# Performance work log

Measured on AMD Instinct MI355X. Metric: run time of the kernel, lower is better.

## Reference

```python
import jax, jax.numpy as jnp
import numpy as np
from jax import lax

B, IMG, P, STRIDE, CIN = 4, 256, 8, 8, 1
D, NH, L = 768, 8, 21
GRID = (IMG - P) // STRIDE + 1  # 32
N = GRID * GRID                 # 1024 tokens
HD = D // NH                    # 96
SCALE = float(HD) ** -0.5


def setup_inputs() -> dict:
    key = jax.random.key(0)
    ks = jax.random.split(key, 9)
    s = 0.02
    return {
        "sam": jax.random.normal(ks[0], (B, CIN, IMG, IMG), dtype=jnp.float32),
        "conv_w": jax.random.normal(ks[1], (D, CIN, P, P), dtype=jnp.float32) * s,
        "conv_b": jnp.zeros((D,), dtype=jnp.float32),
        "ln_g": jnp.ones((D,), dtype=jnp.float32),
        "ln_b": jnp.zeros((D,), dtype=jnp.float32),
        "pos": jax.random.normal(ks[2], (N, D), dtype=jnp.float32) * s,
        "q_w": jax.random.normal(ks[3], (L, D, D), dtype=jnp.float32) * s,
        "kv_w": jax.random.normal(ks[4], (L, D, 2 * D), dtype=jnp.float32) * s,
        "proj_w": jax.random.normal(ks[5], (L, D, D), dtype=jnp.float32) * s,
        "proj_b": jnp.zeros((L, D), dtype=jnp.float32),
    }


def _layernorm(x, g, b, eps=1e-5):
    mu = jnp.mean(x, axis=-1, keepdims=True)
    var = jnp.mean(jnp.square(x - mu), axis=-1, keepdims=True)
    return (x - mu) * lax.rsqrt(var + eps) * g + b


def _guidance(x, qw, kvw, pw, pb):
    b, n, c = x.shape
    q = jnp.einsum('bnc,cd->bnd', x, qw).reshape(b, n, NH, HD).transpose(0, 2, 1, 3)
    kv = jnp.einsum('bnc,cd->bnd', x, kvw)
    k = kv[..., :c].reshape(b, n, NH, HD).transpose(0, 2, 1, 3)
    v = kv[..., c:].reshape(b, n, NH, HD).transpose(0, 2, 1, 3)
    attn = jax.nn.softmax(jnp.einsum('bhnd,bhmd->bhnm', q, k) * SCALE, axis=-1)
    o = jnp.einsum('bhnm,bhmd->bhnd', attn, v).transpose(0, 2, 1, 3).reshape(b, n, c)
    o = jnp.einsum('bnc,cd->bnd', o, pw) + pb
    return o + x  # residual (dropouts are identity in eval)


def reference(sam, conv_w, conv_b, ln_g, ln_b, pos, q_w, kv_w, proj_w, proj_b):
    # Patch embed: conv (valid, stride=patch) -> [B,D,32,32] -> tokens -> LN
    y = lax.conv_general_dilated(sam, conv_w, window_strides=(STRIDE, STRIDE),
                                 padding='VALID',
                                 dimension_numbers=('NCHW', 'OIHW', 'NCHW'))
    y = y + conv_b[None, :, None, None]
    y = y.reshape(B, D, N).transpose(0, 2, 1)  # [B,N,D]
    y = _layernorm(y, ln_g, ln_b)
    x0 = y + pos[None]  # pos_embed(arange) broadcast over batch
    # Faithful to source: each block consumes the SAME x0; output is last block's.
    out = x0
    for i in range(L):
        out = _guidance(x0, q_w[i], kv_w[i], proj_w[i], proj_b[i])
    return out
```

## Files before the change

kernel.cpp:

```cpp
#include <hip/hip_runtime.h>
#include <hip/hip_bf16.h>

typedef __attribute__((ext_vector_type(4))) float f32x4;
typedef __attribute__((ext_vector_type(8))) short s16x8;
typedef unsigned short u16;
typedef unsigned int u32;

#define DEV __device__ __forceinline__

DEV u16 f2bf(float f) {
  union { float f; u32 u; } v; v.f = f;
  u32 r = v.u + 0x7fffu + ((v.u >> 16) & 1u);
  return (u16)(r >> 16);
}

#define MFMA16(a, b, c) __builtin_amdgcn_mfma_f32_16x16x32_bf16((a), (b), (c), 0, 0, 0)
#define GLD16(g, l) __builtin_amdgcn_global_load_lds((const __attribute__((address_space(1))) u32*)(g), (__attribute__((address_space(3))) u32*)(l), 16, 0, 0)

#define QSCALE 0.10206207261596577f

__global__ __launch_bounds__(256) void prep_k(
    const float* __restrict__ qw, const float* __restrict__ kvw,
    const float* __restrict__ pw, u16* __restrict__ wqkvT, u16* __restrict__ pwT,
    const float* __restrict__ sam, const float* __restrict__ cw,
    const float* __restrict__ cb, const float* __restrict__ g,
    const float* __restrict__ bb, const float* __restrict__ pos,
    float* __restrict__ x0f, u16* __restrict__ x0b) {
  __shared__ float tb[32][33];
  __shared__ float pix[4][64];
  __shared__ float red[2][4][4];
  int bid = blockIdx.x;
  if (bid < 2304) {
    int ct = bid / 24, kt = (bid % 24) * 32;
    const float* src;
    u16* dst;
    int ncols, tn, dstbase;
    float scale = 1.0f;
    if (ct < 24) {
      src = qw; ncols = 768; tn = ct * 32; dst = wqkvT; dstbase = tn; scale = QSCALE;
    } else if (ct < 72) {
      src = kvw; ncols = 1536; tn = (ct - 24) * 32; dst = wqkvT; dstbase = 768 + tn;
    } else {
      src = pw; ncols = 768; tn = (ct - 72) * 32; dst = pwT; dstbase = tn;
    }
    int tx = threadIdx.x & 31, ty = threadIdx.x >> 5;
#pragma unroll
    for (int i = 0; i < 4; i++)
      tb[ty + i * 8][tx] = src[(size_t)(kt + ty + i * 8) * ncols + tn + tx];
    __syncthreads();
#pragma unroll
    for (int i = 0; i < 4; i++)
      dst[(size_t)(dstbase + ty + i * 8) * 768 + kt + tx] = f2bf(tb[tx][ty + i * 8] * scale);
    return;
  }
  int blk = bid - 2304;
  int b = blk >> 8, nq = blk & 255;
  int t = threadIdx.x;
  {
    int tk = t >> 6, p = t & 63;
    int n = nq * 4 + tk;
    int gi = n >> 5, gj = n & 31;
    pix[tk][p] = sam[b * 65536 + (gi * 8 + (p >> 3)) * 256 + gj * 8 + (p & 7)];
  }
  __syncthreads();
  float acc[3][4];
#pragma unroll
  for (int u = 0; u < 3; u++) {
    int d = t + u * 256;
    const float4* w4 = (const float4*)(cw + (size_t)d * 64);
    float a0 = cb[d];
    float av0 = a0, av1 = a0, av2 = a0, av3 = a0;
#pragma unroll
    for (int pc = 0; pc < 16; pc++) {
      float4 w = w4[pc];
      av0 += w.x * pix[0][pc * 4] + w.y * pix[0][pc * 4 + 1] + w.z * pix[0][pc * 4 + 2] + w.w * pix[0][pc * 4 + 3];
      av1 += w.x * pix[1][pc * 4] + w.y * pix[1][pc * 4 + 1] + w.z * pix[1][pc * 4 + 2] + w.w * pix[1][pc * 4 + 3];
      av2 += w.x * pix[2][pc * 4] + w.y * pix[2][pc * 4 + 1] + w.z * pix[2][pc * 4 + 2] + w.w * pix[2][pc * 4 + 3];
      av3 += w.x * pix[3][pc * 4] + w.y * pix[3][pc * 4 + 1] + w.z * pix[3][pc * 4 + 2] + w.w * pix[3][pc * 4 + 3];
    }
    acc[u][0] = av0; acc[u][1] = av1; acc[u][2] = av2; acc[u][3] = av3;
  }
  float s1[4], s2[4];
#pragma unroll
  for (int tk = 0; tk < 4; tk++) {
    s1[tk] = acc[0][tk] + acc[1][tk] + acc[2][tk];
    s2[tk] = acc[0][tk] * acc[0][tk] + acc[1][tk] * acc[1][tk] + acc[2][tk] * acc[2][tk];
  }
#pragma unroll
  for (int m = 1; m < 64; m <<= 1) {
#pragma unroll
    for (int tk = 0; tk < 4; tk++) {
      s1[tk] += __shfl_xor(s1[tk], m);
      s2[tk] += __shfl_xor(s2[tk], m);
    }
  }
  int wid = t >> 6;
  if ((t & 63) == 0) {
#pragma unroll
    for (int tk = 0; tk < 4; tk++) { red[0][wid][tk] = s1[tk]; red[1][wid][tk] = s2[tk]; }
  }
  __syncthreads();
  float mu[4], rs[4];
#pragma unroll
  for (int tk = 0; tk < 4; tk++) {
    float S1 = red[0][0][tk] + red[0][1][tk] + red[0][2][tk] + red[0][3][tk];
    float S2 = red[1][0][tk] + red[1][1][tk] + red[1][2][tk] + red[1][3][tk];
    mu[tk] = S1 * (1.0f / 768.0f);
    float var = S2 * (1.0f / 768.0f) - mu[tk] * mu[tk];
    rs[tk] = rsqrtf(var + 1e-5f);
  }
#pragma unroll
  for (int u = 0; u < 3; u++) {
    int d = t + u * 256;
    float gg = g[d], bbv = bb[d];
#pragma unroll
    for (int tk = 0; tk < 4; tk++) {
      int n = nq * 4 + tk;
      float val = (acc[u][tk] - mu[tk]) * rs[tk] * gg + bbv + pos[(size_t)n * 768 + d];
      size_t idx = ((size_t)(b * 1024 + n)) * 768 + d;
      x0f[idx] = val;
      x0b[idx] = f2bf(val);
    }
  }
}

template <int EPI>
__global__ __launch_bounds__(256, 2) void gemm128(
    const u16* __restrict__ A, const u16* __restrict__ BT, int M, int N, int K,
    u16* __restrict__ q, u16* __restrict__ kk_, u16* __restrict__ vt,
    const float* __restrict__ pb, const float* __restrict__ x0f,
    float* __restrict__ outp) {
  __shared__ __align__(16) u16 Al[2][128 * 32];
  __shared__ __align__(16) u16 Bl[2][128 * 32];
  int m0 = blockIdx.y * 128, n0 = blockIdx.x * 128;
  int tid = threadIdx.x, lane = tid & 63, wid = tid >> 6;
  int wr = wid >> 1, wc = wid & 1;
  f32x4 acc[4][4] = {};
  int arow = lane >> 2, acol = (lane & 3) * 8;
  const u16* ag = A + (size_t)(m0 + wid * 32 + arow) * K + acol;
  const u16* bg = BT + (size_t)(n0 + wid * 32 + arow) * K + acol;
  int lofs = wid * 32 * 32;
#define STAGE_G(bufi, kk)                              \
  do {                                                 \
    GLD16(ag + (kk), &Al[bufi][lofs]);                 \
    GLD16(ag + (kk) + 16 * K, &Al[bufi][lofs + 512]);  \
    GLD16(bg + (kk), &Bl[bufi][lofs]);                 \
    GLD16(bg + (kk) + 16 * K, &Bl[bufi][lofs + 512]);  \
  } while (0)
  STAGE_G(0, 0);
  int nk = K >> 5;
  int cur = 0;
  for (int t = 0; t < nk; t++) {
    __syncthreads();
    if (t + 1 < nk) STAGE_G(cur ^ 1, (t + 1) * 32);
    s16x8 af[4], bf[4];
#pragma unroll
    for (int m = 0; m < 4; m++)
      af[m] = *(const s16x8*)&Al[cur][(wr * 64 + m * 16 + (lane & 15)) * 32 + (lane >> 4) * 8];
#pragma unroll
    for (int nn = 0; nn < 4; nn++)
      bf[nn] = *(const s16x8*)&Bl[cur][(wc * 64 + nn * 16 + (lane & 15)) * 32 + (lane >> 4) * 8];
#pragma unroll
    for (int m = 0; m < 4; m++)
#pragma unroll
      for (int nn = 0; nn < 4; nn++)
        acc[m][nn] = MFMA16(af[m], bf[nn], acc[m][nn]);
    cur ^= 1;
  }
#undef STAGE_G
#pragma unroll
  for (int m = 0; m < 4; m++) {
    int rbase = m0 + wr * 64 + m * 16 + ((lane >> 4) << 2);
#pragma unroll
    for (int nn = 0; nn < 4; nn++) {
      int col = n0 + wc * 64 + nn * 16 + (lane & 15);
      f32x4 v = acc[m][nn];
      if (EPI == 0) {
        if (col < 1536) {
          int cc = (col < 768) ? col : col - 768;
          int h = cc / 96, hd = cc % 96;
          u16* dst = (col < 768) ? q : kk_;
          int bq = (rbase >> 10) * 8 + h;
#pragma unroll
          for (int i = 0; i < 4; i++) {
            int row = rbase + i;
            dst[((size_t)bq * 1024 + (row & 1023)) * 96 + hd] = f2bf(v[i]);
          }
        } else {
          int cc = col - 1536;
          int h = cc / 96, hd = cc % 96;
          int bq = (rbase >> 10) * 8 + h;
          ushort4 pk;
          pk.x = f2bf(v[0]); pk.y = f2bf(v[1]); pk.z = f2bf(v[2]); pk.w = f2bf(v[3]);
          *(ushort4*)&vt[((size_t)bq * 96 + hd) * 1024 + (rbase & 1023)] = pk;
        }
      } else {
        float add = pb[col];
#pragma unroll
        for (int i = 0; i < 4; i++) {
          size_t idx = (size_t)(rbase + i) * 768 + col;
          outp[idx] = v[i] + add + x0f[idx];
        }
      }
    }
  }
}

__global__ __launch_bounds__(256, 2) void attn_k(
    const u16* __restrict__ qg, const u16* __restrict__ kg,
    const u16* __restrict__ vg, u16* __restrict__ o) {
  int bh = blockIdx.x >> 3, qb = blockIdx.x & 7;
  int b = bh >> 3, h = bh & 7;
  int tid = threadIdx.x, lane = tid & 63, wid = tid >> 6;
  int q0 = qb * 128 + wid * 32;
  s16x8 aq[2][3];
#pragma unroll
  for (int mf = 0; mf < 2; mf++)
#pragma unroll
    for (int kc = 0; kc < 3; kc++)
      aq[mf][kc] = *(const s16x8*)&qg[((size_t)bh * 1024 + q0 + mf * 16 + (lane & 15)) * 96 + kc * 32 + (lane >> 4) * 8];
  float mrun[2][4], lrun[2][4];
  f32x4 accO[2][6] = {};
#pragma unroll
  for (int mf = 0; mf < 2; mf++)
#pragma unroll
    for (int i = 0; i < 4; i++) { mrun[mf][i] = -1e30f; lrun[mf][i] = 0.0f; }
  __shared__ __align__(16) u16 Kl[64][104];
  __shared__ __align__(16) u16 VTl[96][72];
  __shared__ __align__(16) u16 Pl[4][32][72];
  const u16* kbase = kg + (size_t)bh * 1024 * 96;
  const u16* vbase = vg + (size_t)bh * 96 * 1024;
  int kkey[3], koff[3], vhd[3], vko[3];
#pragma unroll
  for (int it = 0; it < 3; it++) {
    int c = it * 256 + tid;
    kkey[it] = c / 12; koff[it] = (c % 12) * 8;
    vhd[it] = c >> 3;  vko[it] = (c & 7) * 8;
  }
  uint4 kreg[3], vreg[3];
#define ALOAD(kt)                                                                        \
  do {                                                                                   \
    _Pragma("unroll") for (int it = 0; it < 3; it++) {                                   \
      kreg[it] = *(const uint4*)&kbase[(size_t)((kt) * 64 + kkey[it]) * 96 + koff[it]];  \
      vreg[it] = *(const uint4*)&vbase[(size_t)vhd[it] * 1024 + (kt) * 64 + vko[it]];    \
    }                                                                                    \
  } while (0)
#define AWRITE()                                             \
  do {                                                       \
    _Pragma("unroll") for (int it = 0; it < 3; it++) {       \
      *(uint4*)&Kl[kkey[it]][koff[it]] = kreg[it];           \
      *(uint4*)&VTl[vhd[it]][vko[it]] = vreg[it];            \
    }                                                        \
  } while (0)
  ALOAD(0);
  AWRITE();
  for (int kt = 0; kt < 16; kt++) {
    if (kt < 15) ALOAD(kt + 1);
    __syncthreads();
    f32x4 s[2][4] = {};
#pragma unroll
    for (int nf = 0; nf < 4; nf++) {
#pragma unroll
      for (int kc = 0; kc < 3; kc++) {
        s16x8 bk = *(const s16x8*)&Kl[nf * 16 + (lane & 15)][kc * 32 + (lane >> 4) * 8];
        s[0][nf] = MFMA16(aq[0][kc], bk, s[0][nf]);
        s[1][nf] = MFMA16(aq[1][kc], bk, s[1][nf]);
      }
    }
#pragma unroll
    for (int mf = 0; mf < 2; mf++) {
#pragma unroll
      for (int i = 0; i < 4; i++) {
        float rm = fmaxf(fmaxf(s[mf][0][i], s[mf][1][i]), fmaxf(s[mf][2][i], s[mf][3][i]));
#pragma unroll
        for (int m = 1; m < 16; m <<= 1) rm = fmaxf(rm, __shfl_xor(rm, m));
        float newm = fmaxf(mrun[mf][i], rm);
        float alpha = __expf(mrun[mf][i] - newm);
        float ps = 0.0f;
#pragma unroll
        for (int nf = 0; nf < 4; nf++) {
          float p = __expf(s[mf][nf][i] - newm);
          s[mf][nf][i] = p;
          ps += p;
        }
#pragma unroll
        for (int m = 1; m < 16; m <<= 1) ps += __shfl_xor(ps, m);
        lrun[mf][i] = lrun[mf][i] * alpha + ps;
        mrun[mf][i] = newm;
#pragma unroll
        for (int nf = 0; nf < 6; nf++) accO[mf][nf][i] *= alpha;
      }
#pragma unroll
      for (int nf = 0; nf < 4; nf++)
#pragma unroll
        for (int i = 0; i < 4; i++)
          Pl[wid][mf * 16 + ((lane >> 4) << 2) + i][nf * 16 + (lane & 15)] = f2bf(s[mf][nf][i]);
    }
    asm volatile("s_waitcnt lgkmcnt(0)" ::: "memory");
    __builtin_amdgcn_sched_barrier(0);
#pragma unroll
    for (int kc = 0; kc < 2; kc++) {
      s16x8 ap0 = *(const s16x8*)&Pl[wid][0 + (lane & 15)][kc * 32 + (lane >> 4) * 8];
      s16x8 ap1 = *(const s16x8*)&Pl[wid][16 + (lane & 15)][kc * 32 + (lane >> 4) * 8];
#pragma unroll
      for (int nf = 0; nf < 6; nf++) {
        s16x8 bv = *(const s16x8*)&VTl[nf * 16 + (lane & 15)][kc * 32 + (lane >> 4) * 8];
        accO[0][nf] = MFMA16(ap0, bv, accO[0][nf]);
        accO[1][nf] = MFMA16(ap1, bv, accO[1][nf]);
      }
    }
    __syncthreads();
    if (kt < 15) AWRITE();
  }
#undef ALOAD
#undef AWRITE
#pragma unroll
  for (int mf = 0; mf < 2; mf++) {
#pragma unroll
    for (int i = 0; i < 4; i++) {
      float inv = 1.0f / lrun[mf][i];
      int tok = qb * 128 + wid * 32 + mf * 16 + ((lane >> 4) << 2) + i;
      u16* orow = o + ((size_t)(b * 1024 + tok)) * 768 + h * 96;
#pragma unroll
      for (int nf = 0; nf < 6; nf++)
        orow[nf * 16 + (lane & 15)] = f2bf(accO[mf][nf][i] * inv);
    }
  }
}

extern "C" void kernel_launch(void* const* d_in, const int* in_sizes, int n_in,
                              void* d_out, int out_size, void* d_ws, size_t ws_size,
                              hipStream_t stream) {
  const float* sam    = (const float*)d_in[0];
  const float* conv_w = (const float*)d_in[1];
  const float* conv_b = (const float*)d_in[2];
  const float* ln_g   = (const float*)d_in[3];
  const float* ln_b   = (const float*)d_in[4];
  const float* pos    = (const float*)d_in[5];
  const float* q_w    = (const float*)d_in[6] + (size_t)20 * 768 * 768;
  const float* kv_w   = (const float*)d_in[7] + (size_t)20 * 768 * 1536;
  const float* proj_w = (const float*)d_in[8] + (size_t)20 * 768 * 768;
  const float* proj_b = (const float*)d_in[9] + (size_t)20 * 768;

  char* ws = (char*)d_ws;
  float* x0f  = (float*)ws; ws += (size_t)4096 * 768 * 4;
  u16* x0b    = (u16*)ws;   ws += (size_t)4096 * 768 * 2;
  u16* wqkvT  = (u16*)ws;   ws += (size_t)2304 * 768 * 2;
  u16* pwT    = (u16*)ws;   ws += (size_t)768 * 768 * 2;
  u16* qs     = (u16*)ws;   ws += (size_t)32 * 1024 * 96 * 2;
  u16* ks     = (u16*)ws;   ws += (size_t)32 * 1024 * 96 * 2;
  u16* vts    = (u16*)ws;   ws += (size_t)32 * 96 * 1024 * 2;
  u16* ob     = (u16*)ws;   ws += (size_t)4096 * 768 * 2;

  prep_k<<<3328, 256, 0, stream>>>(q_w, kv_w, proj_w, wqkvT, pwT, sam, conv_w,
                                   conv_b, ln_g, ln_b, pos, x0f, x0b);
  dim3 g1(18, 32);
  gemm128<0><<<g1, 256, 0, stream>>>(x0b, wqkvT, 4096, 2304, 768, qs, ks, vts,
                                     nullptr, nullptr, nullptr);
  attn_k<<<256, 256, 0, stream>>>(qs, ks, vts, ob);
  dim3 g2(6, 32);
  gemm128<1><<<g2, 256, 0, stream>>>(ob, pwT, 4096, 768, 768, nullptr, nullptr,
                                     nullptr, proj_b, x0f, (float*)d_out);
}
```

Measured before the change: 356.4 us.

## Restructure attention kernel: smaller query tiles, direct V loads, lazy rescale

The attention kernel now gives each wave 16 query rows instead of 32, and the grid doubles to 512 blocks with a remapped block index so more blocks run across the CUs. V fragments are read straight from global memory into registers instead of being staged through LDS, and the register-prefetch double buffering of K is dropped. The online softmax skips the accumulator rescale when no row maximum increases, and s_setprio is raised around the MFMA sections. The trade-off is less K/V reuse per block, which doubles K/V global traffic, and global-load latency is now exposed on every tile.

```diff
diff --git a/kernel.cpp b/kernel.cpp
--- a/kernel.cpp
+++ b/kernel.cpp
@@ -209,122 +209,113 @@
 __global__ __launch_bounds__(256, 2) void attn_k(
     const u16* __restrict__ qg, const u16* __restrict__ kg,
     const u16* __restrict__ vg, u16* __restrict__ o) {
-  int bh = blockIdx.x >> 3, qb = blockIdx.x & 7;
+  int newid = ((blockIdx.x & 7) << 6) + (blockIdx.x >> 3);
+  int bh = newid >> 4, qb = newid & 15;
   int b = bh >> 3, h = bh & 7;
   int tid = threadIdx.x, lane = tid & 63, wid = tid >> 6;
-  int q0 = qb * 128 + wid * 32;
-  s16x8 aq[2][3];
-#pragma unroll
-  for (int mf = 0; mf < 2; mf++)
-#pragma unroll
-    for (int kc = 0; kc < 3; kc++)
-      aq[mf][kc] = *(const s16x8*)&qg[((size_t)bh * 1024 + q0 + mf * 16 + (lane & 15)) * 96 + kc * 32 + (lane >> 4) * 8];
-  float mrun[2][4], lrun[2][4];
-  f32x4 accO[2][6] = {};
-#pragma unroll
-  for (int mf = 0; mf < 2; mf++)
-#pragma unroll
-    for (int i = 0; i < 4; i++) { mrun[mf][i] = -1e30f; lrun[mf][i] = 0.0f; }
-  __shared__ __align__(16) u16 Kl[64][104];
-  __shared__ __align__(16) u16 VTl[96][72];
-  __shared__ __align__(16) u16 Pl[4][32][72];
+  int l15 = lane & 15, l4 = lane >> 4;
+  int q0 = qb * 64 + wid * 16;
+  const u16* qbase = qg + (size_t)bh * 1024 * 96;
   const u16* kbase = kg + (size_t)bh * 1024 * 96;
   const u16* vbase = vg + (size_t)bh * 96 * 1024;
-  int kkey[3], koff[3], vhd[3], vko[3];
+  s16x8 aq[3];
+#pragma unroll
+  for (int kc = 0; kc < 3; kc++)
+    aq[kc] = *(const s16x8*)&qbase[(size_t)(q0 + l15) * 96 + kc * 32 + l4 * 8];
+  float mrun[4], lrun[4];
+  f32x4 accO[6] = {};
+#pragma unroll
+  for (int i = 0; i < 4; i++) { mrun[i] = -1e30f; lrun[i] = 0.0f; }
+  __shared__ __align__(16) u16 Kl[64][104];
+  __shared__ __align__(16) u16 Pl[4][16][72];
+  int kkey[3], koff[3];
 #pragma unroll
   for (int it = 0; it < 3; it++) {
     int c = it * 256 + tid;
     kkey[it] = c / 12; koff[it] = (c % 12) * 8;
-    vhd[it] = c >> 3;  vko[it] = (c & 7) * 8;
-  }
-  uint4 kreg[3], vreg[3];
-#define ALOAD(kt)                                                                        \
-  do {                                                                                   \
-    _Pragma("unroll") for (int it = 0; it < 3; it++) {                                   \
-      kreg[it] = *(const uint4*)&kbase[(size_t)((kt) * 64 + kkey[it]) * 96 + koff[it]];  \
-      vreg[it] = *(const uint4*)&vbase[(size_t)vhd[it] * 1024 + (kt) * 64 + vko[it]];    \
-    }                                                                                    \
-  } while (0)
-#define AWRITE()                                             \
-  do {                                                       \
-    _Pragma("unroll") for (int it = 0; it < 3; it++) {       \
-      *(uint4*)&Kl[kkey[it]][koff[it]] = kreg[it];           \
-      *(uint4*)&VTl[vhd[it]][vko[it]] = vreg[it];            \
-    }                                                        \
-  } while (0)
-  ALOAD(0);
-  AWRITE();
+  }
   for (int kt = 0; kt < 16; kt++) {
-    if (kt < 15) ALOAD(kt + 1);
+#pragma unroll
+    for (int it = 0; it < 3; it++)
+      *(uint4*)&Kl[kkey[it]][koff[it]] =
+          *(const uint4*)&kbase[(size_t)(kt * 64 + kkey[it]) * 96 + koff[it]];
     __syncthreads();
-    f32x4 s[2][4] = {};
-#pragma unroll
-    for (int nf = 0; nf < 4; nf++) {
+    s16x8 bv[6][2];
+#pragma unroll
+    for (int nf = 0; nf < 6; nf++)
+#pragma unroll
+      for (int kc = 0; kc < 2; kc++)
+        bv[nf][kc] = *(const s16x8*)&vbase[(size_t)(nf * 16 + l15) * 1024 +
+                                           kt * 64 + kc * 32 + l4 * 8];
+    f32x4 s4[4] = {};
+    __builtin_amdgcn_s_setprio(1);
+#pragma unroll
+    for (int nf = 0; nf < 4; nf++)
 #pragma unroll
       for (int kc = 0; kc < 3; kc++) {
-        s16x8 bk = *(const s16x8*)&Kl[nf * 16 + (lane & 15)][kc * 32 + (lane >> 4) * 8];
-        s[0][nf] = MFMA16(aq[0][kc], bk, s[0][nf]);
-        s[1][nf] = MFMA16(aq[1][kc], bk, s[1][nf]);
+        s16x8 bk = *(const s16x8*)&Kl[nf * 16 + l15][kc * 32 + l4 * 8];
+        s4[nf] = MFMA16(aq[kc], bk, s4[nf]);
       }
-    }
-#pragma unroll
-    for (int mf = 0; mf < 2; mf++) {
+    __builtin_amdgcn_s_setprio(0);
+    float rm[4];
+#pragma unroll
+    for (int i = 0; i < 4; i++) {
+      rm[i] = fmaxf(fmaxf(s4[0][i], s4[1][i]), fmaxf(s4[2][i], s4[3][i]));
+#pragma unroll
+      for (int m = 1; m < 16; m <<= 1) rm[i] = fmaxf(rm[i], __shfl_xor(rm[i], m));
+    }
+    bool need = (rm[0] > mrun[0]) || (rm[1] > mrun[1]) ||
+                (rm[2] > mrun[2]) || (rm[3] > mrun[3]);
+    if (__any(need)) {
 #pragma unroll
       for (int i = 0; i < 4; i++) {
-        float rm = fmaxf(fmaxf(s[mf][0][i], s[mf][1][i]), fmaxf(s[mf][2][i], s[mf][3][i]));
-#pragma unroll
-        for (int m = 1; m < 16; m <<= 1) rm = fmaxf(rm, __shfl_xor(rm, m));
-        float newm = fmaxf(mrun[mf][i], rm);
-        float alpha = __expf(mrun[mf][i] - newm);
-        float ps = 0.0f;
-#pragma unroll
-        for (int nf = 0; nf < 4; nf++) {
-          float p = __expf(s[mf][nf][i] - newm);
-          s[mf][nf][i] = p;
-          ps += p;
-        }
-#pragma unroll
-        for (int m = 1; m < 16; m <<= 1) ps += __shfl_xor(ps, m);
-        lrun[mf][i] = lrun[mf][i] * alpha + ps;
-        mrun[mf][i] = newm;
-#pragma unroll
-        for (int nf = 0; nf < 6; nf++) accO[mf][nf][i] *= alpha;
+        float newm = fmaxf(mrun[i], rm[i]);
+        float al = __expf(mrun[i] - newm);
+        mrun[i] = newm;
+        lrun[i] *= al;
+#pragma unroll
+        for (int nf = 0; nf < 6; nf++) accO[nf][i] *= al;
       }
-#pragma unroll
-      for (int nf = 0; nf < 4; nf++)
-#pragma unroll
-        for (int i = 0; i < 4; i++)
-          Pl[wid][mf * 16 + ((lane >> 4) << 2) + i][nf * 16 + (lane & 15)] = f2bf(s[mf][nf][i]);
-    }
+    }
+#pragma unroll
+    for (int i = 0; i < 4; i++) {
+      float ps = 0.0f;
+#pragma unroll
+      for (int nf = 0; nf < 4; nf++) {
+        float p = __expf(s4[nf][i] - mrun[i]);
+        s4[nf][i] = p;
+        ps += p;
+      }
+#pragma unroll
+      for (int m = 1; m < 16; m <<= 1) ps += __shfl_xor(ps, m);
+      lrun[i] += ps;
+    }
+#pragma unroll
+    for (int nf = 0; nf < 4; nf++)
+#pragma unroll
+      for (int i = 0; i < 4; i++)
+        Pl[wid][l4 * 4 + i][nf * 16 + l15] = f2bf(s4[nf][i]);
     asm volatile("s_waitcnt lgkmcnt(0)" ::: "memory");
     __builtin_amdgcn_sched_barrier(0);
+    __builtin_amdgcn_s_setprio(1);
 #pragma unroll
     for (int kc = 0; kc < 2; kc++) {
-      s16x8 ap0 = *(const s16x8*)&Pl[wid][0 + (lane & 15)][kc * 32 + (lane >> 4) * 8];
-      s16x8 ap1 = *(const s16x8*)&Pl[wid][16 + (lane & 15)][kc * 32 + (lane >> 4) * 8];
-#pragma unroll
-      for (int nf = 0; nf < 6; nf++) {
-        s16x8 bv = *(const s16x8*)&VTl[nf * 16 + (lane & 15)][kc * 32 + (lane >> 4) * 8];
-        accO[0][nf] = MFMA16(ap0, bv, accO[0][nf]);
-        accO[1][nf] = MFMA16(ap1, bv, accO[1][nf]);
-      }
-    }
+      s16x8 ap = *(const s16x8*)&Pl[wid][l15][kc * 32 + l4 * 8];
+#pragma unroll
+      for (int nf = 0; nf < 6; nf++)
+        accO[nf] = MFMA16(ap, bv[nf][kc], accO[nf]);
+    }
+    __builtin_amdgcn_s_setprio(0);
     __syncthreads();
-    if (kt < 15) AWRITE();
-  }
-#undef ALOAD
-#undef AWRITE
-#pragma unroll
-  for (int mf = 0; mf < 2; mf++) {
-#pragma unroll
-    for (int i = 0; i < 4; i++) {
-      float inv = 1.0f / lrun[mf][i];
-      int tok = qb * 128 + wid * 32 + mf * 16 + ((lane >> 4) << 2) + i;
-      u16* orow = o + ((size_t)(b * 1024 + tok)) * 768 + h * 96;
-#pragma unroll
-      for (int nf = 0; nf < 6; nf++)
-        orow[nf * 16 + (lane & 15)] = f2bf(accO[mf][nf][i] * inv);
-    }
+  }
+#pragma unroll
+  for (int i = 0; i < 4; i++) {
+    float inv = 1.0f / lrun[i];
+    int tok = q0 + l4 * 4 + i;
+    u16* orow = o + ((size_t)(b * 1024 + tok)) * 768 + h * 96;
+#pragma unroll
+    for (int nf = 0; nf < 6; nf++)
+      orow[nf * 16 + l15] = f2bf(accO[nf][i] * inv);
   }
 }
 
@@ -357,7 +348,7 @@
   dim3 g1(18, 32);
   gemm128<0><<<g1, 256, 0, stream>>>(x0b, wqkvT, 4096, 2304, 768, qs, ks, vts,
                                      nullptr, nullptr, nullptr);
-  attn_k<<<256, 256, 0, stream>>>(qs, ks, vts, ob);
+  attn_k<<<512, 256, 0, stream>>>(qs, ks, vts, ob);
   dim3 g2(6, 32);
   gemm128<1><<<g2, 256, 0, stream>>>(ob, pwT, 4096, 768, 768, nullptr, nullptr,
                                      nullptr, proj_b, x0f, (float*)d_out);
```

New measurement: 337.5 us. 5.3% less time.
